# Performance work log

Measured on AMD Instinct MI355X. Metric: run time of the kernel, lower is better.

Reference implementation:

```python
import jax, jax.numpy as jnp
import numpy as np
import math

D_MODEL = 1024
N_HEADS = 16
D_K = 64
D_V = 64
B = 4
S = 1024


def setup_inputs() -> dict:
    key = jax.random.key(0)
    ks = jax.random.split(key, 11)
    # xavier-ish init scale for projections
    s_in = 1.0 / math.sqrt(D_MODEL)
    return {
        "queries": jax.random.normal(ks[0], (B, S, D_MODEL), jnp.float32),
        "keys": jax.random.normal(ks[1], (B, S, D_MODEL), jnp.float32),
        "values": jax.random.normal(ks[2], (B, S, D_MODEL), jnp.float32),
        "Wq": jax.random.normal(ks[3], (D_MODEL, N_HEADS * D_K), jnp.float32) * s_in,
        "bq": jnp.zeros((N_HEADS * D_K,), jnp.float32),
        "Wk": jax.random.normal(ks[4], (D_MODEL, N_HEADS * D_K), jnp.float32) * s_in,
        "bk": jnp.zeros((N_HEADS * D_K,), jnp.float32),
        "Wv": jax.random.normal(ks[5], (D_MODEL, N_HEADS * D_V), jnp.float32) * s_in,
        "bv": jnp.zeros((N_HEADS * D_V,), jnp.float32),
        "Wo": jax.random.normal(ks[6], (N_HEADS * D_V, D_MODEL), jnp.float32) * (1.0 / math.sqrt(N_HEADS * D_V)),
        "bo": jnp.zeros((D_MODEL,), jnp.float32),
    }


def reference(queries, keys, values, Wq, bq, Wk, bk, Wv, bv, Wo, bo):
    Bq, Sq, _ = queries.shape
    Sk = keys.shape[1]
    scale = 1.0 / math.sqrt(D_K)
    # projections -> [B, S, H, d]
    q = (queries @ Wq + bq).reshape(Bq, Sq, N_HEADS, D_K)
    k = (keys @ Wk + bk).reshape(Bq, Sk, N_HEADS, D_K)
    v = (values @ Wv + bv).reshape(Bq, Sk, N_HEADS, D_V)
    # scaled dot-product attention: scores [B, H, Sq, Sk]
    scores = jnp.einsum("bqhd,bkhd->bhqk", q, k) * scale
    attn = jax.nn.softmax(scores, axis=-1)
    # weighted values -> [B, Sq, H*D_V]
    out = jnp.einsum("bhqk,bkhd->bqhd", attn, v).reshape(Bq, Sq, N_HEADS * D_V)
    return out @ Wo + bo
```

## Files before the change

### kernel.cpp

```cpp
#include <hip/hip_runtime.h>

typedef __bf16 bf16;
typedef __attribute__((ext_vector_type(4))) __bf16 bf16x4;
typedef __attribute__((ext_vector_type(8))) __bf16 bf16x8;
typedef __attribute__((ext_vector_type(4))) float f32x4;

#define D_MODEL 1024
#define NH      16
#define DHEAD   64
#define BATCH   4
#define SLEN    1024
#define MROWS   (BATCH * SLEN)
#define C2SCALE 0.18033688f
#define SOFTMAX_OFF 20.0f

__device__ __forceinline__ void async_load16(const void* g, void* l) {
  __builtin_amdgcn_global_load_lds(
      (const __attribute__((address_space(1))) unsigned int*)g,
      (__attribute__((address_space(3))) unsigned int*)l,
      16, 0, 0);
}

__global__ __launch_bounds__(256) void prep_kernel(
    const float* __restrict__ x0, const float* __restrict__ x1, const float* __restrict__ x2,
    bf16* __restrict__ y0, bf16* __restrict__ y1, bf16* __restrict__ y2, int n,
    const float* __restrict__ w0, const float* __restrict__ w1,
    const float* __restrict__ w2, const float* __restrict__ w3,
    bf16* __restrict__ t0, bf16* __restrict__ t1,
    bf16* __restrict__ t2, bf16* __restrict__ t3)
{
  __shared__ float tile[32][33];
  const int bid = blockIdx.x;
  if (bid < 3 * 4096) {
    const int z = bid >> 12, bx = bid & 4095;
    const float* x; bf16* y;
    switch (z) {
      case 0: x = x0; y = y0; break;
      case 1: x = x1; y = y1; break;
      default: x = x2; y = y2; break;
    }
    int i = (bx * 256 + threadIdx.x) * 4;
    if (i + 3 < n) {
      f32x4 v = *(const f32x4*)(x + i);
      bf16x4 o;
      o[0] = (bf16)v[0]; o[1] = (bf16)v[1]; o[2] = (bf16)v[2]; o[3] = (bf16)v[3];
      *(bf16x4*)(y + i) = o;
    }
  } else {
    const int r = bid - 3 * 4096;
    const int z = r >> 10, rr = r & 1023;
    const float* W; bf16* T;
    switch (z) {
      case 0: W = w0; T = t0; break;
      case 1: W = w1; T = t1; break;
      case 2: W = w2; T = t2; break;
      default: W = w3; T = t3; break;
    }
    const int bx = (rr & 31) * 32, by = (rr >> 5) * 32;
    const int tx = threadIdx.x & 31, ty = threadIdx.x >> 5;
    #pragma unroll
    for (int i = 0; i < 32; i += 8)
      tile[ty + i][tx] = W[(size_t)(by + ty + i) * 1024 + bx + tx];
    __syncthreads();
    #pragma unroll
    for (int i = 0; i < 32; i += 8)
      T[(size_t)(bx + ty + i) * 1024 + by + tx] = (bf16)tile[tx][ty + i];
  }
}

__global__ __launch_bounds__(256) void proj_qkv_kernel(
    const bf16* __restrict__ Xq, const bf16* __restrict__ Xk, const bf16* __restrict__ Xv,
    const bf16* __restrict__ WqT, const bf16* __restrict__ WkT, const bf16* __restrict__ WvT,
    const float* __restrict__ bq, const float* __restrict__ bk, const float* __restrict__ bv,
    bf16* __restrict__ Qh, bf16* __restrict__ Kh, bf16* __restrict__ VTo)
{
  __shared__ bf16 As[2][128 * 32];
  __shared__ bf16 Bs[2][128 * 32];
  const int z = blockIdx.z;
  const bf16 *A, *BT; const float* bias;
  switch (z) {
    case 0: A = Xq; BT = WqT; bias = bq; break;
    case 1: A = Xk; BT = WkT; bias = bk; break;
    default: A = Xv; BT = WvT; bias = bv; break;
  }
  const int t = threadIdx.x;
  const int wave = t >> 6, lane = t & 63;
  const int quad = lane >> 4, l16 = lane & 15;
  const int wr = wave >> 1, wc = wave & 1;
  const int bM = blockIdx.y * 128, bN = blockIdx.x * 128;

  f32x4 acc[4][4] = {};

  auto stage = [&](int buf, int k0) {
    #pragma unroll
    for (int i = 0; i < 2; ++i) {
      const int idx = i * 256 + t;
      const int row = idx >> 2, cg = idx & 3;
      async_load16(A  + (size_t)(bM + row) * D_MODEL + k0 + cg * 8,
                   &As[buf][(i * 256 + wave * 64) * 8]);
      async_load16(BT + (size_t)(bN + row) * D_MODEL + k0 + cg * 8,
                   &Bs[buf][(i * 256 + wave * 64) * 8]);
    }
  };
  auto compute = [&](int buf) {
    bf16x8 af[4], bfr[4];
    #pragma unroll
    for (int i = 0; i < 4; ++i)
      af[i] = *(const bf16x8*)(&As[buf][(wr * 64 + i * 16 + l16) * 32 + quad * 8]);
    #pragma unroll
    for (int j = 0; j < 4; ++j)
      bfr[j] = *(const bf16x8*)(&Bs[buf][(wc * 64 + j * 16 + l16) * 32 + quad * 8]);
    #pragma unroll
    for (int i = 0; i < 4; ++i)
      #pragma unroll
      for (int j = 0; j < 4; ++j)
        acc[i][j] = __builtin_amdgcn_mfma_f32_16x16x32_bf16(af[i], bfr[j], acc[i][j], 0, 0, 0);
  };

  stage(0, 0);
  __syncthreads();
  for (int k0 = 0; k0 < D_MODEL; k0 += 64) {
    stage(1, k0 + 32);
    compute(0);
    __syncthreads();
    if (k0 + 64 < D_MODEL) stage(0, k0 + 64);
    compute(1);
    __syncthreads();
  }

  #pragma unroll
  for (int j = 0; j < 4; ++j) {
    const int col = bN + wc * 64 + j * 16 + l16;
    const int h = col >> 6, d = col & 63;
    const float bv_ = bias[col];
    #pragma unroll
    for (int i = 0; i < 4; ++i) {
      const int row0 = bM + wr * 64 + i * 16 + quad * 4;
      const int b = row0 >> 10, s0 = row0 & 1023;
      if (z == 0) {
        bf16* dst = Qh + ((size_t)(b * NH + h) * SLEN) * DHEAD;
        #pragma unroll
        for (int r = 0; r < 4; ++r)
          dst[(size_t)(s0 + r) * DHEAD + d] = (bf16)((acc[i][j][r] + bv_) * C2SCALE);
      } else if (z == 1) {
        bf16* dst = Kh + ((size_t)(b * NH + h) * SLEN) * DHEAD;
        #pragma unroll
        for (int r = 0; r < 4; ++r)
          dst[(size_t)(s0 + r) * DHEAD + d] = (bf16)(acc[i][j][r] + bv_);
      } else {
        bf16x4 pv;
        #pragma unroll
        for (int r = 0; r < 4; ++r) pv[r] = (bf16)(acc[i][j][r] + bv_);
        *(bf16x4*)(VTo + ((size_t)(b * NH + h) * DHEAD + d) * SLEN + s0) = pv;
      }
    }
  }
}

__global__ __launch_bounds__(256) void out_proj_kernel(
    const bf16* __restrict__ AO, const bf16* __restrict__ WoT,
    const float* __restrict__ bo, float* __restrict__ Out)
{
  __shared__ bf16 As[2][64 * 32];
  __shared__ bf16 Bs[2][128 * 32];
  const int t = threadIdx.x;
  const int wave = t >> 6, lane = t & 63;
  const int quad = lane >> 4, l16 = lane & 15;
  const int wr = wave >> 1, wc = wave & 1;
  const int bM = blockIdx.y * 64, bN = blockIdx.x * 128;

  f32x4 acc[2][4] = {};

  auto stage = [&](int buf, int k0) {
    {
      const int row = t >> 2, cg = t & 3;
      async_load16(AO + (size_t)(bM + row) * D_MODEL + k0 + cg * 8,
                   &As[buf][(wave * 64) * 8]);
    }
    #pragma unroll
    for (int i = 0; i < 2; ++i) {
      const int idx = i * 256 + t;
      const int row = idx >> 2, cg = idx & 3;
      async_load16(WoT + (size_t)(bN + row) * D_MODEL + k0 + cg * 8,
                   &Bs[buf][(i * 256 + wave * 64) * 8]);
    }
  };
  auto compute = [&](int buf) {
    bf16x8 af[2], bfr[4];
    #pragma unroll
    for (int i = 0; i < 2; ++i)
      af[i] = *(const bf16x8*)(&As[buf][(wr * 32 + i * 16 + l16) * 32 + quad * 8]);
    #pragma unroll
    for (int j = 0; j < 4; ++j)
      bfr[j] = *(const bf16x8*)(&Bs[buf][(wc * 64 + j * 16 + l16) * 32 + quad * 8]);
    #pragma unroll
    for (int i = 0; i < 2; ++i)
      #pragma unroll
      for (int j = 0; j < 4; ++j)
        acc[i][j] = __builtin_amdgcn_mfma_f32_16x16x32_bf16(af[i], bfr[j], acc[i][j], 0, 0, 0);
  };

  stage(0, 0);
  __syncthreads();
  for (int k0 = 0; k0 < D_MODEL; k0 += 64) {
    stage(1, k0 + 32);
    compute(0);
    __syncthreads();
    if (k0 + 64 < D_MODEL) stage(0, k0 + 64);
    compute(1);
    __syncthreads();
  }

  #pragma unroll
  for (int j = 0; j < 4; ++j) {
    const int col = bN + wc * 64 + j * 16 + l16;
    const float bv_ = bo[col];
    #pragma unroll
    for (int i = 0; i < 2; ++i) {
      const int row0 = bM + wr * 32 + i * 16 + quad * 4;
      #pragma unroll
      for (int r = 0; r < 4; ++r)
        Out[(size_t)(row0 + r) * D_MODEL + col] = acc[i][j][r] + bv_;
    }
  }
}

#define OCS  68
#define WSEG (32 * OCS)
__global__ __launch_bounds__(256) void attn_kernel(
    const bf16* __restrict__ Q, const bf16* __restrict__ K,
    const bf16* __restrict__ VT, bf16* __restrict__ O)
{
  const int lin = blockIdx.x + (blockIdx.y << 5);
  const int xcd = lin & 7, idx = lin >> 3;
  const int bh = xcd * 8 + (idx >> 5);
  const int qBase = (idx & 31) << 5;
  const int b = bh >> 4, h = bh & 15;

  __shared__ float smem_f[4 * WSEG + 4 * 32];

  const int t = threadIdx.x;
  const int wave = t >> 6, lane = t & 63;
  const int quad = lane >> 4, l16 = lane & 15;
  const int kt0 = wave * 256;

  const bf16* qb = Q  + (size_t)bh * SLEN * DHEAD;
  const bf16* kb = K  + (size_t)bh * SLEN * DHEAD;
  const bf16* vb = VT + (size_t)bh * DHEAD * SLEN;

  bf16x8 qa[2][2];
  #pragma unroll
  for (int g = 0; g < 2; ++g) {
    const bf16* qr = qb + (size_t)(qBase + g * 16 + l16) * DHEAD;
    qa[g][0] = *(const bf16x8*)(qr + quad * 8);
    qa[g][1] = *(const bf16x8*)(qr + 32 + quad * 8);
  }

  f32x4 o_acc[2][4] = {};
  float rs[2][4] = {};

  bf16* Pw = (bf16*)smem_f + wave * (2 * 16 * 72);

  bf16x8 kf0[4], kf1[4];
  #pragma unroll
  for (int jn = 0; jn < 4; ++jn) {
    const bf16* kr = kb + (size_t)(kt0 + jn * 16 + l16) * DHEAD;
    kf0[jn] = *(const bf16x8*)(kr + quad * 8);
    kf1[jn] = *(const bf16x8*)(kr + 32 + quad * 8);
  }

  #pragma unroll
  for (int tt = 0; tt < 4; ++tt) {
    const int kt = kt0 + tt * 64;

    bf16x8 vf0[4], vf1[4];
    #pragma unroll
    for (int jn = 0; jn < 4; ++jn) {
      const bf16* vr = vb + (size_t)(jn * 16 + l16) * SLEN + kt;
      vf0[jn] = *(const bf16x8*)(vr + quad * 8);
      vf1[jn] = *(const bf16x8*)(vr + 32 + quad * 8);
    }
    __builtin_amdgcn_sched_barrier(0);

    f32x4 s[2][4] = {};
    __builtin_amdgcn_s_setprio(1);
    #pragma unroll
    for (int jn = 0; jn < 4; ++jn) {
      s[0][jn] = __builtin_amdgcn_mfma_f32_16x16x32_bf16(qa[0][0], kf0[jn], s[0][jn], 0, 0, 0);
      s[0][jn] = __builtin_amdgcn_mfma_f32_16x16x32_bf16(qa[0][1], kf1[jn], s[0][jn], 0, 0, 0);
      s[1][jn] = __builtin_amdgcn_mfma_f32_16x16x32_bf16(qa[1][0], kf0[jn], s[1][jn], 0, 0, 0);
      s[1][jn] = __builtin_amdgcn_mfma_f32_16x16x32_bf16(qa[1][1], kf1[jn], s[1][jn], 0, 0, 0);
    }
    __builtin_amdgcn_s_setprio(0);

    #pragma unroll
    for (int g = 0; g < 2; ++g) {
      bf16* ps = Pw + g * (16 * 72);
      #pragma unroll
      for (int jn = 0; jn < 4; ++jn)
        #pragma unroll
        for (int r = 0; r < 4; ++r) {
          float p = __builtin_amdgcn_exp2f(s[g][jn][r] - SOFTMAX_OFF);
          rs[g][r] += p;
          ps[(quad * 4 + r) * 72 + jn * 16 + l16] = (bf16)p;
        }
    }

    bf16x8 kn0[4], kn1[4];
    if (tt < 3) {
      #pragma unroll
      for (int jn = 0; jn < 4; ++jn) {
        const bf16* kr = kb + (size_t)(kt + 64 + jn * 16 + l16) * DHEAD;
        kn0[jn] = *(const bf16x8*)(kr + quad * 8);
        kn1[jn] = *(const bf16x8*)(kr + 32 + quad * 8);
      }
      __builtin_amdgcn_sched_barrier(0);
    }

    bf16x8 pa[2][2];
    #pragma unroll
    for (int g = 0; g < 2; ++g) {
      const bf16* ps = Pw + g * (16 * 72);
      pa[g][0] = *(const bf16x8*)(&ps[l16 * 72 + quad * 8]);
      pa[g][1] = *(const bf16x8*)(&ps[l16 * 72 + 32 + quad * 8]);
    }

    __builtin_amdgcn_s_setprio(1);
    #pragma unroll
    for (int jn = 0; jn < 4; ++jn) {
      o_acc[0][jn] = __builtin_amdgcn_mfma_f32_16x16x32_bf16(pa[0][0], vf0[jn], o_acc[0][jn], 0, 0, 0);
      o_acc[0][jn] = __builtin_amdgcn_mfma_f32_16x16x32_bf16(pa[0][1], vf1[jn], o_acc[0][jn], 0, 0, 0);
      o_acc[1][jn] = __builtin_amdgcn_mfma_f32_16x16x32_bf16(pa[1][0], vf0[jn], o_acc[1][jn], 0, 0, 0);
      o_acc[1][jn] = __builtin_amdgcn_mfma_f32_16x16x32_bf16(pa[1][1], vf1[jn], o_acc[1][jn], 0, 0, 0);
    }
    __builtin_amdgcn_s_setprio(0);

    if (tt < 3) {
      #pragma unroll
      for (int jn = 0; jn < 4; ++jn) { kf0[jn] = kn0[jn]; kf1[jn] = kn1[jn]; }
    }
  }

  #pragma unroll
  for (int g = 0; g < 2; ++g)
    #pragma unroll
    for (int r = 0; r < 4; ++r) {
      float v = rs[g][r];
      #pragma unroll
      for (int off = 1; off < 16; off <<= 1)
        v += __shfl_xor(v, off);
      rs[g][r] = v;
    }

  __syncthreads();

  float* oc = smem_f + wave * WSEG;
  float* lc = smem_f + 4 * WSEG + wave * 32;
  #pragma unroll
  for (int g = 0; g < 2; ++g) {
    #pragma unroll
    for (int jn = 0; jn < 4; ++jn)
      #pragma unroll
      for (int r = 0; r < 4; ++r)
        oc[(g * 16 + quad * 4 + r) * OCS + jn * 16 + l16] = o_acc[g][jn][r];
    if (l16 == 0)
      #pragma unroll
      for (int r = 0; r < 4; ++r)
        lc[g * 16 + quad * 4 + r] = rs[g][r];
  }
  __syncthreads();

  const int row = wave * 8 + (lane >> 3);
  const int dbase = (lane & 7) * 8;
  float ltot = smem_f[4 * WSEG + row] + smem_f[4 * WSEG + 32 + row] +
               smem_f[4 * WSEG + 64 + row] + smem_f[4 * WSEG + 96 + row];
  f32x4 a0 = {}, a1 = {};
  #pragma unroll
  for (int w = 0; w < 4; ++w) {
    a0 += *(const f32x4*)&smem_f[w * WSEG + row * OCS + dbase];
    a1 += *(const f32x4*)&smem_f[w * WSEG + row * OCS + dbase + 4];
  }
  const float inv = 1.0f / ltot;
  bf16x8 ov;
  #pragma unroll
  for (int e = 0; e < 4; ++e) { ov[e] = (bf16)(a0[e] * inv); ov[e + 4] = (bf16)(a1[e] * inv); }
  bf16* op = O + ((size_t)b * SLEN + qBase + row) * D_MODEL + h * DHEAD + dbase;
  *(bf16x8*)op = ov;
}

extern "C" void kernel_launch(void* const* d_in, const int* in_sizes, int n_in,
                              void* d_out, int out_size, void* d_ws, size_t ws_size,
                              hipStream_t stream) {
  const float* xq = (const float*)d_in[0];
  const float* xk = (const float*)d_in[1];
  const float* xv = (const float*)d_in[2];
  const float* Wq = (const float*)d_in[3];
  const float* bq = (const float*)d_in[4];
  const float* Wk = (const float*)d_in[5];
  const float* bk = (const float*)d_in[6];
  const float* Wv = (const float*)d_in[7];
  const float* bv = (const float*)d_in[8];
  const float* Wo = (const float*)d_in[9];
  const float* bo = (const float*)d_in[10];
  float* out = (float*)d_out;

  const size_t NX = (size_t)MROWS * D_MODEL;
  const size_t NW = (size_t)D_MODEL * D_MODEL;

  char* ws = (char*)d_ws;
  bf16* AO  = (bf16*)ws;  ws += NX * 2;
  bf16* WoT = (bf16*)ws;  ws += NW * 2;
  bf16* Xq  = (bf16*)ws;  ws += NX * 2;
  bf16* Xk  = (bf16*)ws;  ws += NX * 2;
  bf16* Xv  = (bf16*)ws;  ws += NX * 2;
  bf16* WqT = (bf16*)ws;  ws += NW * 2;
  bf16* WkT = (bf16*)ws;  ws += NW * 2;
  bf16* WvT = (bf16*)ws;  ws += NW * 2;
  bf16* Qh  = (bf16*)ws;  ws += NX * 2;
  bf16* Kh  = (bf16*)ws;  ws += NX * 2;
  bf16* VTb = (bf16*)ws;  ws += NX * 2;

  prep_kernel<<<dim3(3 * 4096 + 4 * 1024), 256, 0, stream>>>(
      xq, xk, xv, Xq, Xk, Xv, (int)NX, Wq, Wk, Wv, Wo, WqT, WkT, WvT, WoT);
  proj_qkv_kernel<<<dim3(8, 32, 3), 256, 0, stream>>>(Xq, Xk, Xv, WqT, WkT, WvT, bq, bk, bv, Qh, Kh, VTb);
  attn_kernel<<<dim3(32, 64), 256, 0, stream>>>(Qh, Kh, VTb, AO);
  out_proj_kernel<<<dim3(8, 64), 256, 0, stream>>>(AO, WoT, bo, out);
}
```

Baseline: 244.8 us.

## Restructure attention to share LDS-staged K/V tiles across waves per query block

```diff
diff --git a/kernel.cpp b/kernel.cpp
--- a/kernel.cpp
+++ b/kernel.cpp
@@ -225,62 +225,68 @@
   }
 }
 
-#define OCS  68
-#define WSEG (32 * OCS)
 __global__ __launch_bounds__(256) void attn_kernel(
     const bf16* __restrict__ Q, const bf16* __restrict__ K,
     const bf16* __restrict__ VT, bf16* __restrict__ O)
 {
-  const int lin = blockIdx.x + (blockIdx.y << 5);
-  const int xcd = lin & 7, idx = lin >> 3;
-  const int bh = xcd * 8 + (idx >> 5);
-  const int qBase = (idx & 31) << 5;
+  __shared__ bf16 Kl[2][64 * 64];
+  __shared__ bf16 Vl[2][64 * 64];
+  __shared__ bf16 Ps[4][2 * 16 * 72];
+
+  const int lin = blockIdx.x + (blockIdx.y << 3);
+  const int xcd = lin & 7, rr = lin >> 3;
+  const int bh = xcd * 8 + (rr >> 3);
+  const int qBase = (rr & 7) << 7;
   const int b = bh >> 4, h = bh & 15;
-
-  __shared__ float smem_f[4 * WSEG + 4 * 32];
 
   const int t = threadIdx.x;
   const int wave = t >> 6, lane = t & 63;
   const int quad = lane >> 4, l16 = lane & 15;
-  const int kt0 = wave * 256;
+  const int swz = (l16 & 7) << 4;
 
   const bf16* qb = Q  + (size_t)bh * SLEN * DHEAD;
   const bf16* kb = K  + (size_t)bh * SLEN * DHEAD;
   const bf16* vb = VT + (size_t)bh * DHEAD * SLEN;
 
+  const int qRow0 = qBase + wave * 32;
+
   bf16x8 qa[2][2];
   #pragma unroll
   for (int g = 0; g < 2; ++g) {
-    const bf16* qr = qb + (size_t)(qBase + g * 16 + l16) * DHEAD;
+    const bf16* qr = qb + (size_t)(qRow0 + g * 16 + l16) * DHEAD;
     qa[g][0] = *(const bf16x8*)(qr + quad * 8);
     qa[g][1] = *(const bf16x8*)(qr + 32 + quad * 8);
   }
 
   f32x4 o_acc[2][4] = {};
   float rs[2][4] = {};
-
-  bf16* Pw = (bf16*)smem_f + wave * (2 * 16 * 72);
-
-  bf16x8 kf0[4], kf1[4];
-  #pragma unroll
-  for (int jn = 0; jn < 4; ++jn) {
-    const bf16* kr = kb + (size_t)(kt0 + jn * 16 + l16) * DHEAD;
-    kf0[jn] = *(const bf16x8*)(kr + quad * 8);
-    kf1[jn] = *(const bf16x8*)(kr + 32 + quad * 8);
-  }
-
-  #pragma unroll
-  for (int tt = 0; tt < 4; ++tt) {
-    const int kt = kt0 + tt * 64;
-
-    bf16x8 vf0[4], vf1[4];
+  bf16* Pw = Ps[wave];
+
+  auto stageTile = [&](int buf, int tile) {
+    const int kt = tile * 64;
+    #pragma unroll
+    for (int i = 0; i < 2; ++i) {
+      const int c = i * 256 + t;
+      const int row = c >> 3;
+      const int sl = ((c & 7) ^ (row & 7)) * 8;
+      async_load16(kb + (size_t)(kt + row) * DHEAD + sl,
+                   &Kl[buf][(i * 256 + wave * 64) * 8]);
+      async_load16(vb + (size_t)row * SLEN + kt + sl,
+                   &Vl[buf][(i * 256 + wave * 64) * 8]);
+    }
+  };
+
+  auto tileCompute = [&](int buf) {
+    const char* kB = (const char*)&Kl[buf][0];
+    const char* vB = (const char*)&Vl[buf][0];
+
+    bf16x8 kf0[4], kf1[4];
     #pragma unroll
     for (int jn = 0; jn < 4; ++jn) {
-      const bf16* vr = vb + (size_t)(jn * 16 + l16) * SLEN + kt;
-      vf0[jn] = *(const bf16x8*)(vr + quad * 8);
-      vf1[jn] = *(const bf16x8*)(vr + 32 + quad * 8);
-    }
-    __builtin_amdgcn_sched_barrier(0);
+      const int rb = (jn * 16 + l16) * 128;
+      kf0[jn] = *(const bf16x8*)(kB + rb + ((quad * 16) ^ swz));
+      kf1[jn] = *(const bf16x8*)(kB + rb + ((64 + quad * 16) ^ swz));
+    }
 
     f32x4 s[2][4] = {};
     __builtin_amdgcn_s_setprio(1);
@@ -306,23 +312,20 @@
         }
     }
 
-    bf16x8 kn0[4], kn1[4];
-    if (tt < 3) {
-      #pragma unroll
-      for (int jn = 0; jn < 4; ++jn) {
-        const bf16* kr = kb + (size_t)(kt + 64 + jn * 16 + l16) * DHEAD;
-        kn0[jn] = *(const bf16x8*)(kr + quad * 8);
-        kn1[jn] = *(const bf16x8*)(kr + 32 + quad * 8);
-      }
-      __builtin_amdgcn_sched_barrier(0);
-    }
-
     bf16x8 pa[2][2];
     #pragma unroll
     for (int g = 0; g < 2; ++g) {
       const bf16* ps = Pw + g * (16 * 72);
       pa[g][0] = *(const bf16x8*)(&ps[l16 * 72 + quad * 8]);
       pa[g][1] = *(const bf16x8*)(&ps[l16 * 72 + 32 + quad * 8]);
+    }
+
+    bf16x8 vf0[4], vf1[4];
+    #pragma unroll
+    for (int jn = 0; jn < 4; ++jn) {
+      const int rb = (jn * 16 + l16) * 128;
+      vf0[jn] = *(const bf16x8*)(vB + rb + ((quad * 16) ^ swz));
+      vf1[jn] = *(const bf16x8*)(vB + rb + ((64 + quad * 16) ^ swz));
     }
 
     __builtin_amdgcn_s_setprio(1);
@@ -334,11 +337,20 @@
       o_acc[1][jn] = __builtin_amdgcn_mfma_f32_16x16x32_bf16(pa[1][1], vf1[jn], o_acc[1][jn], 0, 0, 0);
     }
     __builtin_amdgcn_s_setprio(0);
-
-    if (tt < 3) {
-      #pragma unroll
-      for (int jn = 0; jn < 4; ++jn) { kf0[jn] = kn0[jn]; kf1[jn] = kn1[jn]; }
-    }
+  };
+
+  stageTile(0, 0);
+  __syncthreads();
+
+  #pragma unroll 1
+  for (int tp = 0; tp < 8; ++tp) {
+    const int tt = tp * 2;
+    stageTile(1, tt + 1);
+    tileCompute(0);
+    __syncthreads();
+    if (tt + 2 < 16) stageTile(0, tt + 2);
+    tileCompute(1);
+    __syncthreads();
   }
 
   #pragma unroll
@@ -352,40 +364,17 @@
       rs[g][r] = v;
     }
 
-  __syncthreads();
-
-  float* oc = smem_f + wave * WSEG;
-  float* lc = smem_f + 4 * WSEG + wave * 32;
   #pragma unroll
-  for (int g = 0; g < 2; ++g) {
-    #pragma unroll
-    for (int jn = 0; jn < 4; ++jn)
-      #pragma unroll
-      for (int r = 0; r < 4; ++r)
-        oc[(g * 16 + quad * 4 + r) * OCS + jn * 16 + l16] = o_acc[g][jn][r];
-    if (l16 == 0)
-      #pragma unroll
-      for (int r = 0; r < 4; ++r)
-        lc[g * 16 + quad * 4 + r] = rs[g][r];
-  }
-  __syncthreads();
-
-  const int row = wave * 8 + (lane >> 3);
-  const int dbase = (lane & 7) * 8;
-  float ltot = smem_f[4 * WSEG + row] + smem_f[4 * WSEG + 32 + row] +
-               smem_f[4 * WSEG + 64 + row] + smem_f[4 * WSEG + 96 + row];
-  f32x4 a0 = {}, a1 = {};
-  #pragma unroll
-  for (int w = 0; w < 4; ++w) {
-    a0 += *(const f32x4*)&smem_f[w * WSEG + row * OCS + dbase];
-    a1 += *(const f32x4*)&smem_f[w * WSEG + row * OCS + dbase + 4];
-  }
-  const float inv = 1.0f / ltot;
-  bf16x8 ov;
-  #pragma unroll
-  for (int e = 0; e < 4; ++e) { ov[e] = (bf16)(a0[e] * inv); ov[e + 4] = (bf16)(a1[e] * inv); }
-  bf16* op = O + ((size_t)b * SLEN + qBase + row) * D_MODEL + h * DHEAD + dbase;
-  *(bf16x8*)op = ov;
+  for (int g = 0; g < 2; ++g)
+    #pragma unroll
+    for (int r = 0; r < 4; ++r) {
+      const float inv = 1.0f / rs[g][r];
+      const int row = qRow0 + g * 16 + quad * 4 + r;
+      bf16* op = O + ((size_t)b * SLEN + row) * D_MODEL + h * DHEAD;
+      #pragma unroll
+      for (int jn = 0; jn < 4; ++jn)
+        op[jn * 16 + l16] = (bf16)(o_acc[g][jn][r] * inv);
+    }
 }
 
 extern "C" void kernel_launch(void* const* d_in, const int* in_sizes, int n_in,
@@ -423,6 +412,6 @@
   prep_kernel<<<dim3(3 * 4096 + 4 * 1024), 256, 0, stream>>>(
       xq, xk, xv, Xq, Xk, Xv, (int)NX, Wq, Wk, Wv, Wo, WqT, WkT, WvT, WoT);
   proj_qkv_kernel<<<dim3(8, 32, 3), 256, 0, stream>>>(Xq, Xk, Xv, WqT, WkT, WvT, bq, bk, bv, Qh, Kh, VTb);
-  attn_kernel<<<dim3(32, 64), 256, 0, stream>>>(Qh, Kh, VTb, AO);
+  attn_kernel<<<dim3(8, 64), 256, 0, stream>>>(Qh, Kh, VTb, AO);
   out_proj_kernel<<<dim3(8, 64), 256, 0, stream>>>(AO, WoT, bo, out);
 }
```

Result: faster. 214.9 us (-12.2%).
